# Kernel optimization log

Hardware: AMD Instinct MI355X
Metric: run time of the kernel (lower is better)

## Reference

```python
import jax, jax.numpy as jnp
import numpy as np

T, B, D, H, L = 512, 64, 512, 512, 2  # seq_len, batch, input, hidden, layers (bidirectional)


def _xavier(k, shape):
    fan_out, fan_in = shape
    lim = np.sqrt(6.0 / (fan_in + fan_out)).astype(np.float32)
    return jax.random.uniform(k, shape, minval=-lim, maxval=lim, dtype=jnp.float32)


def setup_inputs() -> dict:
    key = jax.random.key(0)
    ks = jax.random.split(key, 1 + 4 * L)
    inp = {"x": jax.random.normal(ks[0], (T, B, D), dtype=jnp.float32)}
    idx = 1
    for layer in range(L):
        din = D if layer == 0 else 2 * H
        for d in ("f", "b"):
            inp[f"w_ih{layer}_{d}"] = _xavier(ks[idx], (4 * H, din)); idx += 1
            inp[f"w_hh{layer}_{d}"] = _xavier(ks[idx], (4 * H, H)); idx += 1
            # xavier_uniform() in the module fills both biases with forget_bias=1.0
            inp[f"b_ih{layer}_{d}"] = jnp.ones((4 * H,), jnp.float32)
            inp[f"b_hh{layer}_{d}"] = jnp.ones((4 * H,), jnp.float32)
    return inp


def _lstm_dir(x, w_ih, w_hh, b_ih, b_hh, reverse):
    """Run one direction of a VarLSTMCell over time. x: [T,B,Din] -> h: [T,B,H]."""
    hdim = w_hh.shape[1]
    # precompute input contribution for all timesteps (same math as per-step matmul)
    xg = jnp.einsum('tbd,gd->tbg', x, w_ih) + b_ih + b_hh  # [T,B,4H]

    def step(carry, xg_t):
        h, c = carry
        gates = xg_t + h @ w_hh.T  # [B,4H]
        i, f, g, o = jnp.split(gates, 4, axis=-1)  # PyTorch LSTMCell gate order
        c = jax.nn.sigmoid(f) * c + jax.nn.sigmoid(i) * jnp.tanh(g)
        h = jax.nn.sigmoid(o) * jnp.tanh(c)
        return (h, c), h

    init = (jnp.zeros((x.shape[1], hdim), x.dtype), jnp.zeros((x.shape[1], hdim), x.dtype))
    _, hs = jax.lax.scan(step, init, xg, reverse=reverse)
    return hs  # [T,B,H], time-ordered (scan reverse keeps original ordering)


def reference(x,
              w_ih0_f, w_hh0_f, b_ih0_f, b_hh0_f,
              w_ih0_b, w_hh0_b, b_ih0_b, b_hh0_b,
              w_ih1_f, w_hh1_f, b_ih1_f, b_hh1_f,
              w_ih1_b, w_hh1_b, b_ih1_b, b_hh1_b):
    params = [
        ((w_ih0_f, w_hh0_f, b_ih0_f, b_hh0_f), (w_ih0_b, w_hh0_b, b_ih0_b, b_hh0_b)),
        ((w_ih1_f, w_hh1_f, b_ih1_f, b_hh1_f), (w_ih1_b, w_hh1_b, b_ih1_b, b_hh1_b)),
    ]
    out = x
    for fwd_p, bwd_p in params:
        h_f = _lstm_dir(out, *fwd_p, reverse=False)
        h_b = _lstm_dir(out, *bwd_p, reverse=True)
        out = jnp.concatenate([h_f, h_b], axis=-1)  # [T,B,2H]
        # dropout=0.0 -> inter-layer dropout is identity
    return out
```

## Files before the change

kernel.cpp:

```cpp
#include <hip/hip_runtime.h>
#include <hip/hip_bf16.h>
#include <stdint.h>


typedef __attribute__((ext_vector_type(8))) _Float16 half8;
typedef __attribute__((ext_vector_type(4))) float f32x4;
typedef __attribute__((ext_vector_type(4))) uint32_t u32x4;
typedef unsigned long long ull;

#define AS(p, v) __hip_atomic_store((p), (v), __ATOMIC_RELAXED, __HIP_MEMORY_SCOPE_AGENT)

#define TAGMASK 0x4000400040004000ULL
#define TM32    0x40004000u
#define PAT_L1A 0x0000400000004000ULL
#define PAT_L1B 0x4000000040000000ULL
#define PAT_INIT_LO 0x40004000u
#define PAT_INIT_HI 0x00000000u

__device__ __forceinline__ unsigned short f2h(float f) {
    union { _Float16 h; unsigned short u; } c; c.h = (_Float16)f; return c.u;
}
__device__ __forceinline__ float h2f(unsigned short u) {
    union { _Float16 h; unsigned short u; } c; c.u = u; return (float)c.h;
}

__global__ __launch_bounds__(256) void prep_kernel(
    const float* __restrict__ x,
    const float* __restrict__ w0f, const float* __restrict__ w0b,
    const float* __restrict__ w1f, const float* __restrict__ w1b,
    const float* __restrict__ bi0f, const float* __restrict__ bh0f,
    const float* __restrict__ bi0b, const float* __restrict__ bh0b,
    const float* __restrict__ bi1f, const float* __restrict__ bh1f,
    const float* __restrict__ bi1b, const float* __restrict__ bh1b,
    unsigned short* __restrict__ xh,
    unsigned short* __restrict__ wihh,
    float* __restrict__ bias,
    uint32_t* __restrict__ hbufi)
{
    const long total = 5801984L;
    long stride = (long)gridDim.x * blockDim.x;
    for (long i = (long)blockIdx.x * blockDim.x + threadIdx.x; i < total; i += stride) {
        if (i < 4194304L) {
            float4 v = ((const float4*)x)[i];
            ushort4 o; o.x=f2h(v.x); o.y=f2h(v.y); o.z=f2h(v.z); o.w=f2h(v.w);
            ((ushort4*)xh)[i] = o;
        } else if (i < 5767168L) {
            long j = i - 4194304L;
            const float* src; long sq;
            if (j < 262144L)       { src = w0f; sq = j;            }
            else if (j < 524288L)  { src = w0b; sq = j - 262144L;  }
            else if (j < 1048576L) { src = w1f; sq = j - 524288L;  }
            else                   { src = w1b; sq = j - 1048576L; }
            float4 v = ((const float4*)src)[sq];
            ushort4 o; o.x=f2h(v.x); o.y=f2h(v.y); o.z=f2h(v.z); o.w=f2h(v.w);
            ((ushort4*)wihh)[j] = o;
        } else if (i < 5769216L) {
            long j = i - 5767168L;
            int ld = (int)(j >> 9);
            long cq = j & 511L;
            const float* bi = ld==0?bi0f: ld==1?bi0b: ld==2?bi1f:bi1b;
            const float* bh = ld==0?bh0f: ld==1?bh0b: ld==2?bh1f:bh1b;
            float4 a = ((const float4*)bi)[cq];
            float4 b = ((const float4*)bh)[cq];
            float4 o; o.x=a.x+b.x; o.y=a.y+b.y; o.z=a.z+b.z; o.w=a.w+b.w;
            ((float4*)bias)[ld*512 + cq] = o;
        } else {
            long j = i - 5769216L;
            uint4 p; p.x=PAT_INIT_LO; p.y=PAT_INIT_HI; p.z=PAT_INIT_LO; p.w=PAT_INIT_HI;
            ((uint4*)hbufi)[j] = p;
        }
    }
}

__global__ __launch_bounds__(256) void gemm_xg(
    const unsigned short* __restrict__ A,
    const unsigned short* __restrict__ Wf,
    const unsigned short* __restrict__ Wb,
    unsigned short* __restrict__ xg,
    int Din)
{
    __shared__ __align__(16) unsigned short As[4096];
    __shared__ __align__(16) unsigned short Bs[4096];
    const int dir = blockIdx.z;
    const unsigned short* W = dir ? Wb : Wf;
    unsigned short* out = xg + (size_t)dir * 32768 * 2048;
    const int bn = blockIdx.x, bm = blockIdx.y;
    const int tid = threadIdx.x;
    const int wave = tid >> 6, lane = tid & 63;
    const int q = lane >> 4, ln = lane & 15;
    const int wm = wave >> 1, wn = wave & 1;

    f32x4 acc[4][4];
#pragma unroll
    for (int a = 0; a < 4; ++a)
#pragma unroll
        for (int b = 0; b < 4; ++b) acc[a][b] = (f32x4){0.f, 0.f, 0.f, 0.f};

    const int kiter = Din >> 5;
    for (int kb = 0; kb < kiter; ++kb) {
        __syncthreads();
#pragma unroll
        for (int i = 0; i < 2; ++i) {
            int off = i*4096 + wave*1024 + lane*16;
            int row = off >> 6;
            int kel = (off & 63) >> 1;
            const unsigned short* sa = A + (size_t)(bm*128 + row)*Din + kb*32 + kel;
            const unsigned short* sb = W + (size_t)(bn*128 + row)*Din + kb*32 + kel;
            __builtin_amdgcn_global_load_lds(
                (const __attribute__((address_space(1))) uint32_t*)sa,
                (__attribute__((address_space(3))) uint32_t*)((char*)As + i*4096 + wave*1024),
                16, 0, 0);
            __builtin_amdgcn_global_load_lds(
                (const __attribute__((address_space(1))) uint32_t*)sb,
                (__attribute__((address_space(3))) uint32_t*)((char*)Bs + i*4096 + wave*1024),
                16, 0, 0);
        }
        __syncthreads();
        half8 af[4], bf[4];
#pragma unroll
        for (int mt = 0; mt < 4; ++mt)
            af[mt] = *(const half8*)((const char*)As + (wm*64 + mt*16 + ln)*64 + q*16);
#pragma unroll
        for (int nt = 0; nt < 4; ++nt)
            bf[nt] = *(const half8*)((const char*)Bs + (wn*64 + nt*16 + ln)*64 + q*16);
#pragma unroll
        for (int mt = 0; mt < 4; ++mt)
#pragma unroll
            for (int nt = 0; nt < 4; ++nt)
                acc[mt][nt] = __builtin_amdgcn_mfma_f32_16x16x32_f16(af[mt], bf[nt], acc[mt][nt], 0, 0, 0);
    }
    const int tt = bm*2 + wm;
#pragma unroll
    for (int mt = 0; mt < 4; ++mt)
#pragma unroll
        for (int nt = 0; nt < 4; ++nt) {
            int col = bn*128 + wn*64 + nt*16 + ln;
            int gate = col >> 9, colg = col & 511;
            union { unsigned short u[4]; ull v; } p;
#pragma unroll
            for (int r = 0; r < 4; ++r) p.u[r] = f2h(acc[mt][nt][r]);
            __builtin_nontemporal_store(p.v,
                (ull*)(out + (((size_t)tt*4 + gate)*512 + colg)*64 + mt*16 + q*4));
        }
}

struct RecCtx {
    const unsigned short* hbuf_c;
    unsigned short* hbuf;
    unsigned short* outh;
    float* outf;
    int layer, R0, C0, tid, wv, lane, g, wc, ln, q;
    int c0row, colq, wb0, wb1;
    uint32_t ep0, ep1;
    ull pat0, pat1;
};

__device__ __forceinline__ void poll_stage(const RecCtx& cx, int d, int sm1,
                                           unsigned short* lbuf)
{
    const int slot_r = sm1 & 3;
    const uint32_t ep = ((sm1 >> 2) & 1) ? cx.ep1 : cx.ep0;
    const uint32_t* s0 = (const uint32_t*)(cx.hbuf_c
        + ((size_t)(slot_r*2 + d)*64 + cx.R0 + cx.c0row)*512 + cx.colq);
    const uint32_t* s1 = (const uint32_t*)(cx.hbuf_c
        + ((size_t)(slot_r*2 + d)*64 + cx.R0 + cx.c0row + 8)*512 + cx.colq);
    u32x4 r0, r1;
    bool ok = false;
    for (int it = 0; it < (1 << 13) && !ok; ++it) {
        asm volatile(
            "global_load_dwordx4 %0, %2, off sc0 sc1\n\t"
            "global_load_dwordx4 %1, %3, off sc0 sc1\n\t"
            "s_waitcnt vmcnt(0)"
            : "=&v"(r0), "=&v"(r1)
            : "v"(s0), "v"(s1)
            : "memory");
        uint32_t bad = 0;
#pragma unroll
        for (int c = 0; c < 4; ++c) bad |= (r0[c] ^ ep) & TM32;
#pragma unroll
        for (int c = 0; c < 4; ++c) bad |= (r1[c] ^ ep) & TM32;
        ok = (bad == 0);
    }
#pragma unroll
    for (int c = 0; c < 4; ++c) { r0[c] &= ~TM32; r1[c] &= ~TM32; }
    *(u32x4*)((char*)lbuf + cx.wb0) = r0;
    *(u32x4*)((char*)lbuf + cx.wb1) = r1;
}

__device__ __forceinline__ void mfma_phase(const RecCtx& cx,
    const unsigned short* lbuf, const half8* wreg, float* achb)
{
    f32x4 acc = (f32x4){0.f, 0.f, 0.f, 0.f};
    const char* hbase = (const char*)lbuf + cx.ln*1024;
    const int lswz = (cx.ln & 7) << 4;
#pragma unroll
    for (int kk = 0; kk < 16; ++kk) {
        half8 a = *(const half8*)(hbase + ((kk*64 + cx.q*16) ^ lswz));
        acc = __builtin_amdgcn_mfma_f32_16x16x32_f16(a, wreg[kk], acc, 0, 0, 0);
    }
    *(f32x4*)&achb[(cx.wv*16 + cx.ln)*20 + cx.q*4] = acc;
}

__device__ __forceinline__ void pointwise(const RecCtx& cx, int d, int s, int t,
    const ull* xv, float* carr, const float* achb, unsigned short* htb,
    float bv0, float bv1, float bv2, float bv3)
{
    f32x4 a0 = *(const f32x4*)&achb[((0*2 + cx.wc)*16 + cx.ln)*20 + cx.q*4];
    f32x4 a1 = *(const f32x4*)&achb[((1*2 + cx.wc)*16 + cx.ln)*20 + cx.q*4];
    f32x4 a2 = *(const f32x4*)&achb[((2*2 + cx.wc)*16 + cx.ln)*20 + cx.q*4];
    f32x4 a3 = *(const f32x4*)&achb[((3*2 + cx.wc)*16 + cx.ln)*20 + cx.q*4];
    unsigned short hs[4];
#pragma unroll
    for (int r = 0; r < 4; ++r) {
        float gi = a0[r] + h2f((unsigned short)(xv[0] >> (16*r))) + bv0;
        float gf = a1[r] + h2f((unsigned short)(xv[1] >> (16*r))) + bv1;
        float gg = a2[r] + h2f((unsigned short)(xv[2] >> (16*r))) + bv2;
        float go = a3[r] + h2f((unsigned short)(xv[3] >> (16*r))) + bv3;
        float si = 1.f / (1.f + __expf(-gi));
        float sf = 1.f / (1.f + __expf(-gf));
        float so = 1.f / (1.f + __expf(-go));
        float tg = 2.f / (1.f + __expf(-2.f*gg)) - 1.f;
        float c  = sf * carr[r] + si * tg;
        carr[r] = c;
        float th = 2.f / (1.f + __expf(-2.f*c)) - 1.f;
        hs[r] = f2h(so * th);
    }
    unsigned short* ht = htb + cx.wc*256;
#pragma unroll
    for (int r = 0; r < 4; ++r) ht[(cx.q*4 + r)*16 + cx.ln] = hs[r];
    ull hv64 = *(const ull*)(ht + (cx.lane >> 2)*16 + (cx.lane & 3)*4);
    const int row  = cx.R0 + (cx.lane >> 2);
    const int colw = cx.C0 + cx.wc*16 + (cx.lane & 3)*4;

    const int slot_w = s & 3;
    const ull wpat = ((s >> 2) & 1) ? cx.pat1 : cx.pat0;
    AS((ull*)(cx.hbuf + ((size_t)(slot_w*2 + d)*64 + row)*512 + colw), hv64 | wpat);

    if (cx.layer == 0) {
        __builtin_nontemporal_store(hv64,
            (ull*)(cx.outh + ((size_t)t*64 + row)*1024 + d*512 + colw));
    } else {
        union { ull u; unsigned short us[4]; } pu; pu.u = hv64;
        union { ull u; float f[2]; } o0, o1;
        o0.f[0] = h2f(pu.us[0]); o0.f[1] = h2f(pu.us[1]);
        o1.f[0] = h2f(pu.us[2]); o1.f[1] = h2f(pu.us[3]);
        ull* dst = (ull*)(cx.outf + ((size_t)t*64 + row)*1024 + d*512 + colw);
        __builtin_nontemporal_store(o0.u, dst);
        __builtin_nontemporal_store(o1.u, dst + 1);
    }
}

__global__ __launch_bounds__(512, 2) void rec_kernel(
    const unsigned short* __restrict__ xg,
    const float* __restrict__ whhf,
    const float* __restrict__ whhb,
    const float* __restrict__ bias,
    unsigned short* __restrict__ hbuf,
    unsigned short* __restrict__ outh,
    float* __restrict__ outf,
    const int layer)
{
    __shared__ __align__(16) unsigned short h_lds[2][8192];
    __shared__ __align__(16) float accbuf[2][2560];
    __shared__ __align__(16) unsigned short htile[2][512];

    const int bx = blockIdx.x;
    RecCtx cx;
    cx.hbuf_c = hbuf; cx.hbuf = hbuf; cx.outh = outh; cx.outf = outf;
    cx.layer = layer;
    const int bh = bx & 3, cg = bx >> 2;
    cx.R0 = bh * 16; cx.C0 = cg * 32;
    cx.tid = threadIdx.x;
    cx.wv = cx.tid >> 6; cx.lane = cx.tid & 63;
    cx.g = cx.wv >> 1; cx.wc = cx.wv & 1;
    cx.ln = cx.lane & 15; cx.q = cx.lane >> 4;
    cx.pat0 = layer ? PAT_L1A : 0ULL;
    cx.pat1 = layer ? PAT_L1B : TAGMASK;
    cx.ep0 = (uint32_t)(cx.pat0 & 0xffffffffULL);
    cx.ep1 = (uint32_t)(cx.pat1 & 0xffffffffULL);
    cx.c0row = cx.tid >> 6;
    cx.colq  = (cx.tid & 63) * 8;
    cx.wb0 = cx.c0row*1024 + (((cx.tid & 63)*16) ^ ((cx.c0row & 7) << 4));
    cx.wb1 = (cx.c0row + 8)*1024 + (((cx.tid & 63)*16) ^ ((cx.c0row & 7) << 4));

    half8 wregA[16], wregB[16];
    {
        const int wrow = cx.g*512 + cx.C0 + cx.wc*16 + cx.ln;
        const float* srcA = whhf + (size_t)wrow * 512 + cx.q*8;
        const float* srcB = whhb + (size_t)wrow * 512 + cx.q*8;
#pragma unroll
        for (int kk = 0; kk < 16; ++kk) {
            float4 v0 = *(const float4*)(srcA + kk*32);
            float4 v1 = *(const float4*)(srcA + kk*32 + 4);
            union { unsigned short u[8]; half8 v; } p;
            p.u[0]=f2h(v0.x); p.u[1]=f2h(v0.y); p.u[2]=f2h(v0.z); p.u[3]=f2h(v0.w);
            p.u[4]=f2h(v1.x); p.u[5]=f2h(v1.y); p.u[6]=f2h(v1.z); p.u[7]=f2h(v1.w);
            wregA[kk] = p.v;
        }
#pragma unroll
        for (int kk = 0; kk < 16; ++kk) {
            float4 v0 = *(const float4*)(srcB + kk*32);
            float4 v1 = *(const float4*)(srcB + kk*32 + 4);
            union { unsigned short u[8]; half8 v; } p;
            p.u[0]=f2h(v0.x); p.u[1]=f2h(v0.y); p.u[2]=f2h(v0.z); p.u[3]=f2h(v0.w);
            p.u[4]=f2h(v1.x); p.u[5]=f2h(v1.y); p.u[6]=f2h(v1.z); p.u[7]=f2h(v1.w);
            wregB[kk] = p.v;
        }
    }

    const unsigned short* xgdA = xg;
    const unsigned short* xgdB = xg + (size_t)32768 * 2048;
    const int myc = cx.C0 + cx.wc*16 + cx.ln;
    float bvA0 = bias[0*512 + myc],        bvA1 = bias[1*512 + myc];
    float bvA2 = bias[2*512 + myc],        bvA3 = bias[3*512 + myc];
    float bvB0 = bias[2048 + 0*512 + myc], bvB1 = bias[2048 + 1*512 + myc];
    float bvB2 = bias[2048 + 2*512 + myc], bvB3 = bias[2048 + 3*512 + myc];
    float carrA[4] = {0.f,0.f,0.f,0.f}, carrB[4] = {0.f,0.f,0.f,0.f};
    ull xvA[4] = {0,0,0,0}, xvB[4] = {0,0,0,0};
    ull xvAn[4] = {0,0,0,0}, xvBn[4] = {0,0,0,0};

    const size_t xoff = (size_t)bh*16 + cx.q*4;

    {
        f32x4 z = (f32x4){0.f,0.f,0.f,0.f};
        *(f32x4*)&accbuf[0][(cx.wv*16 + cx.ln)*20 + cx.q*4] = z;
        *(f32x4*)&accbuf[1][(cx.wv*16 + cx.ln)*20 + cx.q*4] = z;
        __syncthreads();
        if (cx.g == 0) {
#pragma unroll
            for (int k = 0; k < 4; ++k) {
                xvA[k] = __builtin_nontemporal_load(
                    (const ull*)(xgdA + ((size_t)(0*4 + k)*512 + myc)*64 + xoff));
                xvB[k] = __builtin_nontemporal_load(
                    (const ull*)(xgdB + ((size_t)(511*4 + k)*512 + myc)*64 + xoff));
            }
            pointwise(cx, 0, 0, 0,   xvA, carrA, accbuf[0], htile[0], bvA0,bvA1,bvA2,bvA3);
            pointwise(cx, 1, 0, 511, xvB, carrB, accbuf[1], htile[1], bvB0,bvB1,bvB2,bvB3);
#pragma unroll
            for (int k = 0; k < 4; ++k) {
                xvA[k] = __builtin_nontemporal_load(
                    (const ull*)(xgdA + ((size_t)(1*4 + k)*512 + myc)*64 + xoff));
                xvB[k] = __builtin_nontemporal_load(
                    (const ull*)(xgdB + ((size_t)(510*4 + k)*512 + myc)*64 + xoff));
            }
        }
    }

#pragma unroll 1
    for (int s = 1; s < 512; ++s) {
        const int tA = s, tB = 511 - s;

        poll_stage(cx, 0, s - 1, h_lds[0]);
        __syncthreads();
        if (cx.g == 0 && s < 511) {
#pragma unroll
            for (int k = 0; k < 4; ++k) {
                xvAn[k] = __builtin_nontemporal_load(
                    (const ull*)(xgdA + ((size_t)((s+1)*4 + k)*512 + myc)*64 + xoff));
                xvBn[k] = __builtin_nontemporal_load(
                    (const ull*)(xgdB + ((size_t)((510-s)*4 + k)*512 + myc)*64 + xoff));
            }
        }
        mfma_phase(cx, h_lds[0], wregA, accbuf[0]);
        __syncthreads();
        if (cx.g == 0)
            pointwise(cx, 0, s, tA, xvA, carrA, accbuf[0], htile[0], bvA0,bvA1,bvA2,bvA3);

        poll_stage(cx, 1, s - 1, h_lds[1]);
        __syncthreads();
        mfma_phase(cx, h_lds[1], wregB, accbuf[1]);
        __syncthreads();
        if (cx.g == 0) {
            pointwise(cx, 1, s, tB, xvB, carrB, accbuf[1], htile[1], bvB0,bvB1,bvB2,bvB3);
#pragma unroll
            for (int k = 0; k < 4; ++k) { xvA[k] = xvAn[k]; xvB[k] = xvBn[k]; }
        }
    }
}

extern "C" void kernel_launch(void* const* d_in, const int* in_sizes, int n_in,
                              void* d_out, int out_size, void* d_ws, size_t ws_size,
                              hipStream_t stream)
{
    (void)in_sizes; (void)n_in; (void)out_size; (void)ws_size;
    const float* x       = (const float*)d_in[0];
    const float* w_ih0_f = (const float*)d_in[1];
    const float* w_hh0_f = (const float*)d_in[2];
    const float* b_ih0_f = (const float*)d_in[3];
    const float* b_hh0_f = (const float*)d_in[4];
    const float* w_ih0_b = (const float*)d_in[5];
    const float* w_hh0_b = (const float*)d_in[6];
    const float* b_ih0_b = (const float*)d_in[7];
    const float* b_hh0_b = (const float*)d_in[8];
    const float* w_ih1_f = (const float*)d_in[9];
    const float* w_hh1_f = (const float*)d_in[10];
    const float* b_ih1_f = (const float*)d_in[11];
    const float* b_hh1_f = (const float*)d_in[12];
    const float* w_ih1_b = (const float*)d_in[13];
    const float* w_hh1_b = (const float*)d_in[14];
    const float* b_ih1_b = (const float*)d_in[15];
    const float* b_hh1_b = (const float*)d_in[16];

    char* ws = (char*)d_ws;
    unsigned short* xg    = (unsigned short*)(ws + 0);
    unsigned short* wihh  = (unsigned short*)(ws + 268435456L);
    float*          bias  = (float*)         (ws + 281018368L);
    unsigned short* hbuf  = (unsigned short*)(ws + 281051136L);

    unsigned short* in1 = (unsigned short*)d_out;
    unsigned short* xh  = (unsigned short*)((char*)d_out + 67108864L);
    float* outf = (float*)d_out;

    prep_kernel<<<dim3(1024), dim3(256), 0, stream>>>(
        x, w_ih0_f, w_ih0_b, w_ih1_f, w_ih1_b,
        b_ih0_f, b_hh0_f, b_ih0_b, b_hh0_b,
        b_ih1_f, b_hh1_f, b_ih1_b, b_hh1_b,
        xh, wihh, bias, (uint32_t*)hbuf);

    gemm_xg<<<dim3(16, 256, 2), dim3(256), 0, stream>>>(
        xh, wihh, wihh + 1048576, xg, 512);
    rec_kernel<<<dim3(64), dim3(512), 0, stream>>>(
        xg, w_hh0_f, w_hh0_b, bias, hbuf, in1, (float*)nullptr, 0);

    gemm_xg<<<dim3(16, 256, 2), dim3(256), 0, stream>>>(
        in1, wihh + 2097152, wihh + 4194304, xg, 1024);
    rec_kernel<<<dim3(64), dim3(512), 0, stream>>>(
        xg, w_hh1_f, w_hh1_b, bias + 4096, hbuf,
        (unsigned short*)nullptr, outf, 1);
}
```

Before: 5.106 ms.

## Issue both directions' hidden-state polls up front, overlapping backward poll with forward compute

Each timestep now issues the global loads for both the forward and backward hidden-state tiles at once. The forward tile is waited on with a partial vmcnt, so the backward tile's latency hides behind the forward MFMA and pointwise phases. A retry loop runs only when the tag check shows stale data. The block-to-tile mapping also changes so that consecutive blocks share a batch slice instead of a column group. The risks: the hand-counted vmcnt values depend on how many loads the pointwise code issues, the early backward read is more likely to see stale tags and force retries, and removing the s<511 guard makes the last step prefetch xg out of bounds.

```diff
diff --git a/kernel.cpp b/kernel.cpp
--- a/kernel.cpp
+++ b/kernel.cpp
@@ -155,32 +155,34 @@
     ull pat0, pat1;
 };
 
-__device__ __forceinline__ void poll_stage(const RecCtx& cx, int d, int sm1,
-                                           unsigned short* lbuf)
-{
-    const int slot_r = sm1 & 3;
-    const uint32_t ep = ((sm1 >> 2) & 1) ? cx.ep1 : cx.ep0;
-    const uint32_t* s0 = (const uint32_t*)(cx.hbuf_c
-        + ((size_t)(slot_r*2 + d)*64 + cx.R0 + cx.c0row)*512 + cx.colq);
-    const uint32_t* s1 = (const uint32_t*)(cx.hbuf_c
-        + ((size_t)(slot_r*2 + d)*64 + cx.R0 + cx.c0row + 8)*512 + cx.colq);
-    u32x4 r0, r1;
-    bool ok = false;
-    for (int it = 0; it < (1 << 13) && !ok; ++it) {
-        asm volatile(
-            "global_load_dwordx4 %0, %2, off sc0 sc1\n\t"
-            "global_load_dwordx4 %1, %3, off sc0 sc1\n\t"
-            "s_waitcnt vmcnt(0)"
-            : "=&v"(r0), "=&v"(r1)
-            : "v"(s0), "v"(s1)
-            : "memory");
-        uint32_t bad = 0;
-#pragma unroll
-        for (int c = 0; c < 4; ++c) bad |= (r0[c] ^ ep) & TM32;
-#pragma unroll
-        for (int c = 0; c < 4; ++c) bad |= (r1[c] ^ ep) & TM32;
-        ok = (bad == 0);
-    }
+__device__ __forceinline__ uint32_t tagbad(const u32x4& r0, const u32x4& r1, uint32_t ep)
+{
+    uint32_t bad = 0;
+#pragma unroll
+    for (int c = 0; c < 4; ++c) bad |= (r0[c] ^ ep) & TM32;
+#pragma unroll
+    for (int c = 0; c < 4; ++c) bad |= (r1[c] ^ ep) & TM32;
+    return bad;
+}
+
+__device__ __forceinline__ void retry_poll(u32x4& r0, u32x4& r1,
+    const uint32_t* a0, uint32_t ep)
+{
+    asm volatile("s_waitcnt vmcnt(0)" : "+v"(r0), "+v"(r1) :: "memory");
+    uint32_t bad = tagbad(r0, r1, ep);
+    for (int it = 0; bad && it < (1 << 13); ++it) {
+        asm volatile("global_load_dwordx4 %0, %2, off sc0 sc1\n\t"
+                     "global_load_dwordx4 %1, %3, off sc0 sc1\n\t"
+                     "s_waitcnt vmcnt(0)"
+                     : "+v"(r0), "+v"(r1)
+                     : "v"(a0), "v"(a0 + 2048) : "memory");
+        bad = tagbad(r0, r1, ep);
+    }
+}
+
+__device__ __forceinline__ void stage_lds(const RecCtx& cx, u32x4 r0, u32x4 r1,
+                                          unsigned short* lbuf)
+{
 #pragma unroll
     for (int c = 0; c < 4; ++c) { r0[c] &= ~TM32; r1[c] &= ~TM32; }
     *(u32x4*)((char*)lbuf + cx.wb0) = r0;
@@ -268,7 +270,7 @@
     RecCtx cx;
     cx.hbuf_c = hbuf; cx.hbuf = hbuf; cx.outh = outh; cx.outf = outf;
     cx.layer = layer;
-    const int bh = bx & 3, cg = bx >> 2;
+    const int cg = bx & 15, bh = bx >> 4;
     cx.R0 = bh * 16; cx.C0 = cg * 32;
     cx.tid = threadIdx.x;
     cx.wv = cx.tid >> 6; cx.lane = cx.tid & 63;
@@ -349,10 +351,28 @@
 #pragma unroll 1
     for (int s = 1; s < 512; ++s) {
         const int tA = s, tB = 511 - s;
-
-        poll_stage(cx, 0, s - 1, h_lds[0]);
-        __syncthreads();
-        if (cx.g == 0 && s < 511) {
+        const int slot_r = (s - 1) & 3;
+        const uint32_t ep = (((s - 1) >> 2) & 1) ? cx.ep1 : cx.ep0;
+        const uint32_t* pa = (const uint32_t*)(cx.hbuf_c
+            + ((size_t)(slot_r*2 + 0)*64 + cx.R0 + cx.c0row)*512 + cx.colq);
+        const uint32_t* pb = (const uint32_t*)(cx.hbuf_c
+            + ((size_t)(slot_r*2 + 1)*64 + cx.R0 + cx.c0row)*512 + cx.colq);
+
+        u32x4 rA0, rA1, rB0, rB1;
+        asm volatile("global_load_dwordx4 %0, %4, off sc0 sc1\n\t"
+                     "global_load_dwordx4 %1, %5, off sc0 sc1\n\t"
+                     "global_load_dwordx4 %2, %6, off sc0 sc1\n\t"
+                     "global_load_dwordx4 %3, %7, off sc0 sc1"
+                     : "=&v"(rA0), "=&v"(rA1), "=&v"(rB0), "=&v"(rB1)
+                     : "v"(pa), "v"(pa + 2048), "v"(pb), "v"(pb + 2048)
+                     : "memory");
+        asm volatile("s_waitcnt vmcnt(2)" : "+v"(rA0), "+v"(rA1) :: "memory");
+        if (__builtin_expect(tagbad(rA0, rA1, ep) != 0, 0))
+            retry_poll(rA0, rA1, pa, ep);
+        stage_lds(cx, rA0, rA1, h_lds[0]);
+        __syncthreads();
+
+        if (cx.g == 0) {
 #pragma unroll
             for (int k = 0; k < 4; ++k) {
                 xvAn[k] = __builtin_nontemporal_load(
@@ -366,7 +386,15 @@
         if (cx.g == 0)
             pointwise(cx, 0, s, tA, xvA, carrA, accbuf[0], htile[0], bvA0,bvA1,bvA2,bvA3);
 
-        poll_stage(cx, 1, s - 1, h_lds[1]);
+        if (cx.g == 0) {
+            if (layer == 0) asm volatile("s_waitcnt vmcnt(10)" : "+v"(rB0), "+v"(rB1) :: "memory");
+            else            asm volatile("s_waitcnt vmcnt(11)" : "+v"(rB0), "+v"(rB1) :: "memory");
+        } else {
+            asm volatile("s_waitcnt vmcnt(0)"  : "+v"(rB0), "+v"(rB1) :: "memory");
+        }
+        if (__builtin_expect(tagbad(rB0, rB1, ep) != 0, 0))
+            retry_poll(rB0, rB1, pb, ep);
+        stage_lds(cx, rB0, rB1, h_lds[1]);
         __syncthreads();
         mfma_phase(cx, h_lds[1], wregB, accbuf[1]);
         __syncthreads();
```

Result: no change. 5.103 ms (-0.1%).
